# Optimization experiments

Measured on AMD Instinct MI355X. Metric: run time of the kernel, lower is better.

Reference implementation:

```python
import jax, jax.numpy as jnp
import numpy as np

# 8 fixed 3x3 shift-and-subtract kernels (center -1, one neighbor +1)
_KERNELS = np.array([
    [[1, 0, 0], [0, -1, 0], [0, 0, 0]],
    [[0, 1, 0], [0, -1, 0], [0, 0, 0]],
    [[0, 0, 1], [0, -1, 0], [0, 0, 0]],
    [[0, 0, 0], [1, -1, 0], [0, 0, 0]],
    [[0, 0, 0], [0, -1, 1], [0, 0, 0]],
    [[0, 0, 0], [0, -1, 0], [1, 0, 0]],
    [[0, 0, 0], [0, -1, 0], [0, 1, 0]],
    [[0, 0, 0], [0, -1, 0], [0, 0, 1]],
], dtype=np.float32)  # [8,3,3]


def contrast_depth_conv(x):
    # x: [B, H, W] single-channel depth map.
    # torch does groups=8 depthwise conv on the input broadcast to 8 channels,
    # which is identical to a 1->8 channel VALID conv with the 8 kernels.
    w = jnp.asarray(_KERNELS)[:, None, :, :]  # [8,1,3,3] OIHW
    y = jax.lax.conv_general_dilated(
        x[:, None, :, :],  # [B,1,H,W] NCHW
        w,
        window_strides=(1, 1),
        padding='VALID',
        dimension_numbers=('NCHW', 'OIHW', 'NCHW'),
    )
    return y  # [B, 8, H-2, W-2]


def setup_inputs() -> dict:
    key = jax.random.key(0)
    k1, k2 = jax.random.split(key)
    B, H, W = 16384, 32, 32
    out = jax.random.normal(k1, (B, H, W), dtype=jnp.float32)
    label = jax.random.normal(k2, (B, H, W), dtype=jnp.float32)
    return {"out": out, "label": label}


def reference(out, label):
    c_out = contrast_depth_conv(out)      # [B,8,30,30]
    c_label = contrast_depth_conv(label)  # [B,8,30,30]
    diff = c_out - c_label
    return jnp.mean(diff * diff)
```

## Files before the change

### kernel.cpp

```cpp
#include <hip/hip_runtime.h>


#define NBLOCKS 2048
#define THREADS 256

__global__ __launch_bounds__(THREADS, 4) void cdl_partial(
    const float* __restrict__ outp,
    const float* __restrict__ labp,
    float* __restrict__ partial,
    int nimg)
{
    __shared__ __align__(16) float d[32][34];
    __shared__ float red[THREADS / 64];

    const int t = threadIdx.x;
    float acc = 0.f;

    for (int b = blockIdx.x; b < nimg; b += gridDim.x) {
        const float4 ov = ((const float4*)outp)[b * 256 + t];
        const float4 lv = ((const float4*)labp)[b * 256 + t];
        const int row = t >> 3;
        const int col = (t & 7) << 2;
        float2* dst = (float2*)&d[row][col];
        dst[0] = make_float2(ov.x - lv.x, ov.y - lv.y);
        dst[1] = make_float2(ov.z - lv.z, ov.w - lv.w);
        __syncthreads();

        #pragma unroll
        for (int k = 0; k < 2; ++k) {
            const int g = t + k * THREADS;
            if (g < 450) {
                const int y  = g / 15 + 1;
                const int xp = (g % 15) * 2 + 1;
                const float2* r0 = (const float2*)&d[y - 1][xp - 1];
                const float2* r1 = (const float2*)&d[y    ][xp - 1];
                const float2* r2 = (const float2*)&d[y + 1][xp - 1];
                const float2 a0 = r0[0], b0 = r0[1];
                const float2 a1 = r1[0], b1 = r1[1];
                const float2 a2 = r2[0], b2 = r2[1];
                float v;
                const float c0 = a1.y;
                v = a0.x - c0; acc += v * v;
                v = a0.y - c0; acc += v * v;
                v = b0.x - c0; acc += v * v;
                v = a1.x - c0; acc += v * v;
                v = b1.x - c0; acc += v * v;
                v = a2.x - c0; acc += v * v;
                v = a2.y - c0; acc += v * v;
                v = b2.x - c0; acc += v * v;
                const float c1 = b1.x;
                v = a0.y - c1; acc += v * v;
                v = b0.x - c1; acc += v * v;
                v = b0.y - c1; acc += v * v;
                v = a1.y - c1; acc += v * v;
                v = b1.y - c1; acc += v * v;
                v = a2.y - c1; acc += v * v;
                v = b2.x - c1; acc += v * v;
                v = b2.y - c1; acc += v * v;
            }
        }
        __syncthreads();
    }

    #pragma unroll
    for (int off = 32; off; off >>= 1) acc += __shfl_down(acc, off, 64);
    const int lane = t & 63, wid = t >> 6;
    if (lane == 0) red[wid] = acc;
    __syncthreads();
    if (t == 0) partial[blockIdx.x] = red[0] + red[1] + red[2] + red[3];
}

__global__ __launch_bounds__(THREADS) void cdl_final(
    const float* __restrict__ partial,
    float* __restrict__ out,
    float inv_count)
{
    __shared__ float red[THREADS / 64];
    const int t = threadIdx.x;
    float acc = 0.f;
    #pragma unroll
    for (int i = 0; i < NBLOCKS / THREADS; ++i) acc += partial[t + i * THREADS];
    #pragma unroll
    for (int off = 32; off; off >>= 1) acc += __shfl_down(acc, off, 64);
    if ((t & 63) == 0) red[t >> 6] = acc;
    __syncthreads();
    if (t == 0) out[0] = (red[0] + red[1] + red[2] + red[3]) * inv_count;
}

extern "C" void kernel_launch(void* const* d_in, const int* in_sizes, int n_in,
                              void* d_out, int out_size, void* d_ws, size_t ws_size,
                              hipStream_t stream) {
    const float* outp = (const float*)d_in[0];
    const float* labp = (const float*)d_in[1];
    float* partial = (float*)d_ws;
    const int nimg = in_sizes[0] / 1024;
    const float inv_count = 1.0f / ((float)nimg * 8.0f * 900.0f);

    cdl_partial<<<NBLOCKS, THREADS, 0, stream>>>(outp, labp, partial, nimg);
    cdl_final<<<1, THREADS, 0, stream>>>(partial, (float*)d_out, inv_count);
}
```

Before: 28.88 us.

## Assign one image per wavefront with direct global 4x4 patch loads, drop LDS staging

After: 30.61 us. 6.0% more time.

```diff
diff --git a/kernel.cpp b/kernel.cpp
--- a/kernel.cpp
+++ b/kernel.cpp
@@ -1,70 +1,71 @@
 #include <hip/hip_runtime.h>
 
 
-#define NBLOCKS 2048
 #define THREADS 256
 
-__global__ __launch_bounds__(THREADS, 4) void cdl_partial(
+__global__ __launch_bounds__(THREADS) void cdl_partial(
     const float* __restrict__ outp,
     const float* __restrict__ labp,
     float* __restrict__ partial,
     int nimg)
 {
-    __shared__ __align__(16) float d[32][34];
-    __shared__ float red[THREADS / 64];
+    const int t    = threadIdx.x;
+    const int lane = t & 63;
+    const int wid  = t >> 6;
+    const int img  = blockIdx.x * 4 + wid;
 
-    const int t = threadIdx.x;
     float acc = 0.f;
 
-    for (int b = blockIdx.x; b < nimg; b += gridDim.x) {
-        const float4 ov = ((const float4*)outp)[b * 256 + t];
-        const float4 lv = ((const float4*)labp)[b * 256 + t];
-        const int row = t >> 3;
-        const int col = (t & 7) << 2;
-        float2* dst = (float2*)&d[row][col];
-        dst[0] = make_float2(ov.x - lv.x, ov.y - lv.y);
-        dst[1] = make_float2(ov.z - lv.z, ov.w - lv.w);
-        __syncthreads();
+    if (img < nimg) {
+        const float* ob = outp + img * 1024;
+        const float* lb = labp + img * 1024;
 
         #pragma unroll
-        for (int k = 0; k < 2; ++k) {
-            const int g = t + k * THREADS;
-            if (g < 450) {
-                const int y  = g / 15 + 1;
-                const int xp = (g % 15) * 2 + 1;
-                const float2* r0 = (const float2*)&d[y - 1][xp - 1];
-                const float2* r1 = (const float2*)&d[y    ][xp - 1];
-                const float2* r2 = (const float2*)&d[y + 1][xp - 1];
-                const float2 a0 = r0[0], b0 = r0[1];
-                const float2 a1 = r1[0], b1 = r1[1];
-                const float2 a2 = r2[0], b2 = r2[1];
-                float v;
-                const float c0 = a1.y;
-                v = a0.x - c0; acc += v * v;
-                v = a0.y - c0; acc += v * v;
-                v = b0.x - c0; acc += v * v;
-                v = a1.x - c0; acc += v * v;
-                v = b1.x - c0; acc += v * v;
-                v = a2.x - c0; acc += v * v;
-                v = a2.y - c0; acc += v * v;
-                v = b2.x - c0; acc += v * v;
-                const float c1 = b1.x;
-                v = a0.y - c1; acc += v * v;
-                v = b0.x - c1; acc += v * v;
-                v = b0.y - c1; acc += v * v;
-                v = a1.y - c1; acc += v * v;
-                v = b1.y - c1; acc += v * v;
-                v = a2.y - c1; acc += v * v;
-                v = b2.x - c1; acc += v * v;
-                v = b2.y - c1; acc += v * v;
+        for (int i = 0; i < 4; ++i) {
+            const int task = i * 64 + lane;
+            if (task < 225) {
+                const int qy = task / 15;
+                const int qx = task - qy * 15;
+                const int y = 2 * qy + 1;
+                const int x = 2 * qx + 1;
+                const int base = (y - 1) * 32 + (x - 1);
+
+                float dd[4][4];
+                #pragma unroll
+                for (int r = 0; r < 4; ++r) {
+                    const float2 o0 = *(const float2*)(ob + base + r * 32);
+                    const float2 o1 = *(const float2*)(ob + base + r * 32 + 2);
+                    const float2 l0 = *(const float2*)(lb + base + r * 32);
+                    const float2 l1 = *(const float2*)(lb + base + r * 32 + 2);
+                    dd[r][0] = o0.x - l0.x;
+                    dd[r][1] = o0.y - l0.y;
+                    dd[r][2] = o1.x - l1.x;
+                    dd[r][3] = o1.y - l1.y;
+                }
+
+                #pragma unroll
+                for (int cy = 0; cy < 2; ++cy) {
+                    #pragma unroll
+                    for (int cx = 0; cx < 2; ++cx) {
+                        const float c = dd[cy + 1][cx + 1];
+                        #pragma unroll
+                        for (int ny = 0; ny < 3; ++ny) {
+                            #pragma unroll
+                            for (int nx = 0; nx < 3; ++nx) {
+                                if (ny == 1 && nx == 1) continue;
+                                const float v = dd[cy + ny][cx + nx] - c;
+                                acc += v * v;
+                            }
+                        }
+                    }
+                }
             }
         }
-        __syncthreads();
     }
 
     #pragma unroll
     for (int off = 32; off; off >>= 1) acc += __shfl_down(acc, off, 64);
-    const int lane = t & 63, wid = t >> 6;
+    __shared__ float red[4];
     if (lane == 0) red[wid] = acc;
     __syncthreads();
     if (t == 0) partial[blockIdx.x] = red[0] + red[1] + red[2] + red[3];
@@ -73,13 +74,13 @@
 __global__ __launch_bounds__(THREADS) void cdl_final(
     const float* __restrict__ partial,
     float* __restrict__ out,
+    int np,
     float inv_count)
 {
     __shared__ float red[THREADS / 64];
     const int t = threadIdx.x;
     float acc = 0.f;
-    #pragma unroll
-    for (int i = 0; i < NBLOCKS / THREADS; ++i) acc += partial[t + i * THREADS];
+    for (int i = t; i < np; i += THREADS) acc += partial[i];
     #pragma unroll
     for (int off = 32; off; off >>= 1) acc += __shfl_down(acc, off, 64);
     if ((t & 63) == 0) red[t >> 6] = acc;
@@ -94,8 +95,9 @@
     const float* labp = (const float*)d_in[1];
     float* partial = (float*)d_ws;
     const int nimg = in_sizes[0] / 1024;
+    const int nblocks = (nimg + 3) / 4;
     const float inv_count = 1.0f / ((float)nimg * 8.0f * 900.0f);
 
-    cdl_partial<<<NBLOCKS, THREADS, 0, stream>>>(outp, labp, partial, nimg);
-    cdl_final<<<1, THREADS, 0, stream>>>(partial, (float*)d_out, inv_count);
+    cdl_partial<<<nblocks, THREADS, 0, stream>>>(outp, labp, partial, nimg);
+    cdl_final<<<1, THREADS, 0, stream>>>(partial, (float*)d_out, nblocks, inv_count);
 }
```
